# Kernel tuning notes

Hardware: AMD Instinct MI355X
Metric: run time of the kernel (lower is better)

The kernel has to match this reference:

```python
import jax, jax.numpy as jnp
import numpy as np

ANCHORS = np.array([[116.0, 90.0], [156.0, 198.0], [373.0, 326.0]], dtype=np.float32)
IMAGE_SIZE = 2048.0
IGNORE_THRES = 0.5
OBJ_SCALE = 100.0
NO_OBJ_SCALE = 1.0
EPS = 1e-16
BCE_EPS = 1e-12


def _wh_iou(anchors, gwh):
    # anchors: [A,2], gwh: [T,2] -> iou [A,T]
    aw, ah = anchors[:, 0:1], anchors[:, 1:2]            # [A,1]
    gw, gh = gwh[None, :, 0], gwh[None, :, 1]            # [1,T]
    inter = jnp.minimum(aw, gw) * jnp.minimum(ah, gh)
    union = aw * ah + gw * gh - inter
    return inter / (union + EPS)


def _bbox_iou_xywh(box1, box2):
    # boxes [T,4] in (cx, cy, w, h)
    b1x1, b1x2 = box1[:, 0] - box1[:, 2] / 2, box1[:, 0] + box1[:, 2] / 2
    b1y1, b1y2 = box1[:, 1] - box1[:, 3] / 2, box1[:, 1] + box1[:, 3] / 2
    b2x1, b2x2 = box2[:, 0] - box2[:, 2] / 2, box2[:, 0] + box2[:, 2] / 2
    b2y1, b2y2 = box2[:, 1] - box2[:, 3] / 2, box2[:, 1] + box2[:, 3] / 2
    iw = jnp.clip(jnp.minimum(b1x2, b2x2) - jnp.maximum(b1x1, b2x1), 0.0)
    ih = jnp.clip(jnp.minimum(b1y2, b2y2) - jnp.maximum(b1y1, b2y1), 0.0)
    inter = iw * ih
    a1 = (b1x2 - b1x1) * (b1y2 - b1y1)
    a2 = (b2x2 - b2x1) * (b2y2 - b2y1)
    return inter / (a1 + a2 - inter + EPS)


def _masked_mean(v, m):
    return jnp.sum(v * m) / jnp.maximum(jnp.sum(m), 1.0)


def setup_inputs() -> dict:
    key = jax.random.key(0)
    k1, k2, k3 = jax.random.split(key, 3)
    B, A, G, T = 32, 3, 256, 4096
    x = jax.random.normal(k1, (B, A * 5, G, G), jnp.float32) * 0.1
    tb = jax.random.randint(k2, (T, 1), 0, B).astype(jnp.float32)
    tcls = jnp.zeros((T, 1), jnp.float32)
    txywh = jax.random.uniform(k3, (T, 4), jnp.float32, 0.02, 0.98)
    targets = jnp.concatenate([tb, tcls, txywh], axis=1)
    return {"x": x, "targets": targets}


def reference(x, targets):
    B, G = x.shape[0], x.shape[2]
    A = ANCHORS.shape[0]
    stride = IMAGE_SIZE / G

    pred = x.reshape(B, A, 5, G, G).transpose(0, 1, 3, 4, 2)  # [B,A,G,G,5]
    cx = jax.nn.sigmoid(pred[..., 0])
    cy = jax.nn.sigmoid(pred[..., 1])
    w = pred[..., 2]
    h = pred[..., 3]
    pred_conf = jax.nn.sigmoid(pred[..., 4])

    grid_x = jnp.arange(G, dtype=jnp.float32).reshape(1, 1, 1, G)
    grid_y = jnp.arange(G, dtype=jnp.float32).reshape(1, 1, G, 1)
    anchors = jnp.asarray(ANCHORS) / stride                      # [A,2]
    aw = anchors[:, 0].reshape(1, A, 1, 1)
    ah = anchors[:, 1].reshape(1, A, 1, 1)

    pred_boxes = jnp.stack(
        [grid_x + cx, grid_y + cy, jnp.exp(w) * aw, jnp.exp(h) * ah], axis=-1
    )  # [B,A,G,G,4]
    output = jnp.concatenate(
        [pred_boxes.reshape(B, -1, 4) * stride, pred_conf.reshape(B, -1, 1)], axis=-1
    )

    # ---- build_targets (YOLOv3) ----
    tbox = targets[:, 2:6] * G                                   # [T,4] grid units
    gxy, gwh = tbox[:, :2], tbox[:, 2:]
    ious = _wh_iou(anchors, gwh)                                 # [A,T]
    best_n = jnp.argmax(ious, axis=0)                            # [T]
    b = targets[:, 0].astype(jnp.int32)
    gi = jnp.clip(jnp.floor(gxy[:, 0]), 0, G - 1).astype(jnp.int32)
    gj = jnp.clip(jnp.floor(gxy[:, 1]), 0, G - 1).astype(jnp.int32)

    zeros = jnp.zeros((B, A, G, G), jnp.float32)
    obj_mask = zeros.at[b, best_n, gj, gi].set(1.0)
    no_obj_mask = jnp.ones((B, A, G, G), jnp.float32).at[b, best_n, gj, gi].set(0.0)
    aidx = jnp.arange(A)
    keep = (ious.T <= IGNORE_THRES).astype(jnp.float32)          # [T,A]
    no_obj_mask = no_obj_mask.at[
        b[:, None], aidx[None, :], gj[:, None], gi[:, None]
    ].min(keep)

    tx = zeros.at[b, best_n, gj, gi].set(gxy[:, 0] - gi.astype(jnp.float32))
    ty = zeros.at[b, best_n, gj, gi].set(gxy[:, 1] - gj.astype(jnp.float32))
    tw = zeros.at[b, best_n, gj, gi].set(jnp.log(gwh[:, 0] / anchors[best_n, 0] + EPS))
    th = zeros.at[b, best_n, gj, gi].set(jnp.log(gwh[:, 1] / anchors[best_n, 1] + EPS))
    tconf = obj_mask

    pbt = pred_boxes[b, best_n, gj, gi]                          # [T,4]
    iou_scores = zeros.at[b, best_n, gj, gi].set(_bbox_iou_xywh(pbt, tbox))

    # ---- losses ----
    loss_x = _masked_mean((cx - tx) ** 2, obj_mask)
    loss_y = _masked_mean((cy - ty) ** 2, obj_mask)
    loss_w = _masked_mean((w - tw) ** 2, obj_mask)
    loss_h = _masked_mean((h - th) ** 2, obj_mask)
    loss_bbox = loss_x + loss_y + loss_w + loss_h
    bce = -(tconf * jnp.log(pred_conf + BCE_EPS)
            + (1.0 - tconf) * jnp.log(1.0 - pred_conf + BCE_EPS))
    loss_conf_obj = _masked_mean(bce, obj_mask)
    loss_conf_no_obj = _masked_mean(bce, no_obj_mask)
    loss_conf = OBJ_SCALE * loss_conf_obj + NO_OBJ_SCALE * loss_conf_no_obj
    loss_layer = loss_bbox + loss_conf

    # ---- metrics (side-effect scalars in torch; returned stop_gradient'd) ----
    conf50 = (pred_conf > 0.5).astype(jnp.float32)
    iou50 = (iou_scores > 0.5).astype(jnp.float32)
    iou75 = (iou_scores > 0.75).astype(jnp.float32)
    detected = conf50 * tconf
    conf_obj = _masked_mean(pred_conf, obj_mask)
    conf_no_obj = _masked_mean(pred_conf, no_obj_mask)
    precision = jnp.sum(iou50 * detected) / (jnp.sum(conf50) + EPS)
    recall50 = jnp.sum(iou50 * detected) / (jnp.sum(obj_mask) + EPS)
    recall75 = jnp.sum(iou75 * detected) / (jnp.sum(obj_mask) + EPS)
    metrics = jax.lax.stop_gradient(jnp.stack([
        loss_x, loss_y, loss_w, loss_h, loss_bbox, loss_conf, loss_layer,
        conf_obj, conf_no_obj, precision, recall50, recall75,
    ]))
    return output, loss_layer, metrics
```

## Files before the change

### kernel.cpp

```cpp
#include <hip/hip_runtime.h>
#include <cmath>

#define NA 3
#define HSIZE 8192
#define HMASK (HSIZE - 1)

typedef float v4f __attribute__((ext_vector_type(4)));


__device__ __forceinline__ float sigf(float v){ return 1.0f/(1.0f + expf(-v)); }
__device__ __forceinline__ float fast_sig(float v){
  return __builtin_amdgcn_rcpf(1.0f + __expf(-v));
}
__device__ __forceinline__ unsigned hslot(unsigned key){
  return (key * 2654435761u) >> 19;
}

__global__ __launch_bounds__(256) void k_zero(int* __restrict__ p, int n){
  int i = blockIdx.x*256 + threadIdx.x;
  if (i < n) p[i] = 0;
}

__global__ __launch_bounds__(256) void k_targets(
    const float* __restrict__ targets, int T, int G, float stride,
    int* __restrict__ ocell, int* __restrict__ keyarr,
    int* __restrict__ A_key, int* __restrict__ A_val,
    int* __restrict__ B_key, int* __restrict__ B_bits, int* __restrict__ B_maxt)
{
  int t = blockIdx.x*256 + threadIdx.x;
  if (t >= T) return;
  const float* tr = targets + (size_t)t*6;
  int b = (int)tr[0];
  float gx = tr[2]*(float)G, gy = tr[3]*(float)G, gw = tr[4]*(float)G, gh = tr[5]*(float)G;
  float aw[NA] = {116.0f/stride, 156.0f/stride, 373.0f/stride};
  float ah[NA] = { 90.0f/stride, 198.0f/stride, 326.0f/stride};
  float best_iou = -1.0f; int best = 0; int bits = 0;
  #pragma unroll
  for (int a = 0; a < NA; ++a){
    float inter = fminf(aw[a], gw) * fminf(ah[a], gh);
    float uni   = aw[a]*ah[a] + gw*gh - inter;
    float iou   = inter / (uni + 1e-16f);
    if (iou > best_iou){ best_iou = iou; best = a; }
    if (iou > 0.5f) bits |= (1 << a);
  }
  bits |= (1 << best);
  int gi = (int)floorf(gx); gi = gi < 0 ? 0 : (gi > G-1 ? G-1 : gi);
  int gj = (int)floorf(gy); gj = gj < 0 ? 0 : (gj > G-1 ? G-1 : gj);
  int cell = (b*G + gj)*G + gi;
  int okey = cell*4 + best;
  ocell[t]  = okey;
  keyarr[t] = (cell << 3) | bits;

  unsigned s = hslot((unsigned)okey) & HMASK;
  for (;;){
    int prev = atomicCAS(&A_key[s], 0, okey+1);
    if (prev == 0 || prev == okey+1){ atomicMax(&A_val[s], t+1); break; }
    s = (s+1) & HMASK;
  }
  s = hslot((unsigned)cell) & HMASK;
  for (;;){
    int prev = atomicCAS(&B_key[s], 0, cell+1);
    if (prev == 0 || prev == cell+1){
      atomicOr(&B_bits[s], bits);
      atomicMax(&B_maxt[s], t+1);
      break;
    }
    s = (s+1) & HMASK;
  }
}

__global__ __launch_bounds__(256) void k_main(
    const float* __restrict__ x, const float* __restrict__ targets,
    float* __restrict__ out, double* __restrict__ sums,
    int T, int G, float stride, int total_cells, int nblkT,
    const int* __restrict__ ocell, const int* __restrict__ keyarr,
    const int* __restrict__ A_key, const int* __restrict__ A_val,
    const int* __restrict__ B_key, const int* __restrict__ B_bits,
    const int* __restrict__ B_maxt)
{
  __shared__ float lds[256*41];
  __shared__ double sred[4][12];
  int tid = threadIdx.x;
  int lane = tid & 63, wv = tid >> 6;

  if ((int)blockIdx.x < nblkT){
    int t = blockIdx.x*256 + tid;
    double v[12];
    #pragma unroll
    for (int k = 0; k < 12; ++k) v[k] = 0.0;

    if (t < T){
      const float* tr = targets + (size_t)t*6;
      int b = (int)tr[0];
      float gx = tr[2]*(float)G, gy = tr[3]*(float)G, gw = tr[4]*(float)G, gh = tr[5]*(float)G;
      int okey = ocell[t];
      int myk  = keyarr[t];
      int cell = myk >> 3;
      int best = okey & 3;
      int gi = cell % G;
      int gj = (cell / G) % G;
      int GG = G*G;

      unsigned s = hslot((unsigned)okey) & HMASK;
      while (A_key[s] != okey+1) s = (s+1) & HMASK;
      bool owner = (A_val[s] == t+1);

      if (owner){
        float awb = (best==0 ? 116.0f : (best==1 ? 156.0f : 373.0f)) / stride;
        float ahb = (best==0 ?  90.0f : (best==1 ? 198.0f : 326.0f)) / stride;
        const float* xp = x + ((size_t)(b*(NA*5) + best*5))*GG + (size_t)gj*G + gi;
        float x0 = xp[0], x1 = xp[(size_t)GG], x2 = xp[(size_t)2*GG],
              x3 = xp[(size_t)3*GG], x4 = xp[(size_t)4*GG];
        float cx = sigf(x0), cy = sigf(x1), w = x2, h = x3, conf = sigf(x4);
        float tx = gx - (float)gi, ty = gy - (float)gj;
        float tw = logf(gw/awb + 1e-16f), th = logf(gh/ahb + 1e-16f);
        v[3] = (double)((cx-tx)*(cx-tx));
        v[4] = (double)((cy-ty)*(cy-ty));
        v[5] = (double)((w-tw)*(w-tw));
        v[6] = (double)((h-th)*(h-th));
        v[7] = (double)(-logf(conf + 1e-12f));
        v[8] = (double)conf;
        float px = (float)gi + cx, py = (float)gj + cy;
        float pw = expf(w)*awb, ph = expf(h)*ahb;
        float iw = fminf(px + pw*0.5f, gx + gw*0.5f) - fmaxf(px - pw*0.5f, gx - gw*0.5f);
        float ih = fminf(py + ph*0.5f, gy + gh*0.5f) - fmaxf(py - ph*0.5f, gy - gh*0.5f);
        iw = fmaxf(iw, 0.0f); ih = fmaxf(ih, 0.0f);
        float inter = iw*ih;
        float iou = inter / (pw*ph + gw*gh - inter + 1e-16f);
        bool det = conf > 0.5f;
        v[9]  = (iou > 0.5f  && det) ? 1.0 : 0.0;
        v[10] = (iou > 0.75f && det) ? 1.0 : 0.0;
        v[11] = 1.0;
      }

      s = hslot((unsigned)cell) & HMASK;
      while (B_key[s] != cell+1) s = (s+1) & HMASK;
      if (B_maxt[s] == t+1){
        int bits = B_bits[s];
        #pragma unroll
        for (int a = 0; a < NA; ++a){
          if (bits & (1 << a)){
            float x4 = x[((size_t)(b*(NA*5) + a*5 + 4))*GG + (size_t)gj*G + gi];
            float conf = sigf(x4);
            v[0] += (double)(-logf(1.0f - conf + 1e-12f));
            v[1] += (double)conf;
            v[2] += 1.0;
          }
        }
      }
    }

    #pragma unroll
    for (int k = 0; k < 12; ++k){
      #pragma unroll
      for (int off = 32; off > 0; off >>= 1) v[k] += __shfl_down(v[k], off);
    }
    if (lane == 0){
      #pragma unroll
      for (int k = 0; k < 12; ++k) sred[wv][k] = v[k];
    }
    __syncthreads();
    if (tid < 12){
      double sm = sred[0][tid] + sred[1][tid] + sred[2][tid] + sred[3][tid];
      unsafeAtomicAdd(&sums[3 + tid], sm);
    }
  } else {
    int dblk = blockIdx.x - nblkT;
    int i = dblk*256 + tid;
    int cell = i*8;
    float nb = 0.0f, cs = 0.0f; int c50 = 0;

    if (cell < total_cells){
      int GG = G*G;
      int gx    = cell % G;
      int row   = cell / G;
      int gy    = row % G;
      int plane = row / G;
      int a     = plane % NA;
      float aw = (a==0 ? 116.0f : (a==1 ? 156.0f : 373.0f)) / stride;
      float ah = (a==0 ?  90.0f : (a==1 ? 198.0f : 326.0f)) / stride;

      size_t base = (size_t)plane*5*GG + (size_t)gy*G + gx;
      v4f p[5][2];
      #pragma unroll
      for (int c = 0; c < 5; ++c){
        const v4f* pp = (const v4f*)(x + base + (size_t)c*GG);
        p[c][0] = pp[0];
        p[c][1] = pp[1];
      }

      float* myl = lds + tid*41;
      #pragma unroll
      for (int j = 0; j < 8; ++j){
        float cx   = fast_sig(p[0][j>>2][j&3]);
        float cy   = fast_sig(p[1][j>>2][j&3]);
        float pw   = __expf(p[2][j>>2][j&3])*aw;
        float ph   = __expf(p[3][j>>2][j&3])*ah;
        float conf = fast_sig(p[4][j>>2][j&3]);
        myl[j*5+0] = ((float)(gx + j) + cx)*stride;
        myl[j*5+1] = ((float)gy + cy)*stride;
        myl[j*5+2] = pw*stride;
        myl[j*5+3] = ph*stride;
        myl[j*5+4] = conf;
        nb -= __logf(1.0f - conf + 1e-12f);
        cs += conf;
        c50 += (conf > 0.5f) ? 1 : 0;
      }
    }
    __syncthreads();

    {
      size_t waveBase = ((size_t)dblk*2048 + (size_t)wv*512)*5;
      if (waveBase < (size_t)total_cells*5){
        const float* wl = lds + (size_t)(wv*64)*41;
        #pragma unroll
        for (int c = 0; c < 10; ++c){
          int f = (c*64 + lane)*4;
          int owner = f / 40;
          int within = f - owner*40;
          const float* src = wl + owner*41 + within;
          v4f val;
          val.x = src[0]; val.y = src[1]; val.z = src[2]; val.w = src[3];
          __builtin_nontemporal_store(val, (v4f*)(out + waveBase + f));
        }
      }
    }

    float vals[3] = {nb, cs, (float)c50};
    #pragma unroll
    for (int k = 0; k < 3; ++k){
      #pragma unroll
      for (int off = 32; off > 0; off >>= 1) vals[k] += __shfl_down(vals[k], off);
    }
    if (lane == 0){
      sred[wv][0] = (double)vals[0];
      sred[wv][1] = (double)vals[1];
      sred[wv][2] = (double)vals[2];
    }
    __syncthreads();
    if (tid < 3){
      double sm = sred[0][tid] + sred[1][tid] + sred[2][tid] + sred[3][tid];
      unsafeAtomicAdd(&sums[tid], sm);
    }
  }
}

__global__ __launch_bounds__(64) void k_final(
    const double* __restrict__ sums, float* __restrict__ tail, double total_cells)
{
  if (threadIdx.x != 0) return;
  double nb_all = sums[0], conf_all = sums[1], c50_all = sums[2];
  double enb = sums[3], econf = sums[4], ecnt = sums[5];
  double lx = sums[6], ly = sums[7], lw = sums[8], lh = sums[9];
  double bce = sums[10], cobj = sums[11], i50 = sums[12], i75 = sums[13], nobj = sums[14];

  double dObj = fmax(nobj, 1.0);
  double n_noobj = total_cells - ecnt;
  double dNo  = fmax(n_noobj, 1.0);

  double loss_x = lx/dObj, loss_y = ly/dObj, loss_w = lw/dObj, loss_h = lh/dObj;
  double loss_bbox = loss_x + loss_y + loss_w + loss_h;
  double loss_conf_obj   = bce/dObj;
  double loss_conf_noobj = (nb_all - enb)/dNo;
  double loss_conf  = 100.0*loss_conf_obj + 1.0*loss_conf_noobj;
  double loss_layer = loss_bbox + loss_conf;
  double conf_obj   = cobj/dObj;
  double conf_noobj = (conf_all - econf)/dNo;
  double precision  = i50/(c50_all + 1e-16);
  double recall50   = i50/(nobj + 1e-16);
  double recall75   = i75/(nobj + 1e-16);

  tail[0]  = (float)loss_layer;
  tail[1]  = (float)loss_x;
  tail[2]  = (float)loss_y;
  tail[3]  = (float)loss_w;
  tail[4]  = (float)loss_h;
  tail[5]  = (float)loss_bbox;
  tail[6]  = (float)loss_conf;
  tail[7]  = (float)loss_layer;
  tail[8]  = (float)conf_obj;
  tail[9]  = (float)conf_noobj;
  tail[10] = (float)precision;
  tail[11] = (float)recall50;
  tail[12] = (float)recall75;
}

extern "C" void kernel_launch(void* const* d_in, const int* in_sizes, int n_in,
                              void* d_out, int out_size, void* d_ws, size_t ws_size,
                              hipStream_t stream) {
  const float* x       = (const float*)d_in[0];
  const float* targets = (const float*)d_in[1];
  float* out = (float*)d_out;

  const int B = 32;
  int GG = in_sizes[0] / (B * NA * 5);
  int G = (int)(sqrt((double)GG) + 0.5);
  int T = in_sizes[1] / 6;
  float stride = 2048.0f / (float)G;

  char* ws = (char*)d_ws;
  double* sums  = (double*)ws;
  int* A_key  = (int*)(ws + 128);
  int* A_val  = A_key + HSIZE;
  int* B_key  = A_val + HSIZE;
  int* B_bits = B_key + HSIZE;
  int* B_maxt = B_bits + HSIZE;
  int* ocell  = B_maxt + HSIZE;
  int* keyarr = ocell + T;

  int total_cells = B * NA * GG;
  int nzero = 32 + 5*HSIZE;
  int nblkZ = (nzero + 255) / 256;
  int nblkT = (T + 255) / 256;
  int nblkD = (total_cells + 2047) / 2048;

  k_zero   <<<nblkZ, 256, 0, stream>>>((int*)ws, nzero);
  k_targets<<<nblkT, 256, 0, stream>>>(targets, T, G, stride, ocell, keyarr,
                                       A_key, A_val, B_key, B_bits, B_maxt);
  k_main   <<<nblkT + nblkD, 256, 0, stream>>>(x, targets, out, sums,
                                       T, G, stride, total_cells, nblkT,
                                       ocell, keyarr,
                                       A_key, A_val, B_key, B_bits, B_maxt);
  k_final  <<<1, 64, 0, stream>>>(sums, out + (size_t)total_cells*5, (double)total_cells);
}
```

Baseline: 241.7 us.

## Split dense-cell work into two 4-cell halves with per-wave LDS staging

Each thread now handles two groups of 4 consecutive cells, 1024 cells apart, instead of 8 contiguous cells. Both groups' loads are issued up front, and each half is transposed through a smaller per-wave LDS buffer and stored in turn. The block-wide __syncthreads is replaced by wave barriers, which should cut LDS footprint, raise occupancy and make global reads more coalesced. In exchange there are more store phases, extra index arithmetic, and a reliance on wave-local synchronisation being sufficient.

```diff
diff --git a/kernel.cpp b/kernel.cpp
--- a/kernel.cpp
+++ b/kernel.cpp
@@ -78,7 +78,7 @@
     const int* __restrict__ B_key, const int* __restrict__ B_bits,
     const int* __restrict__ B_maxt)
 {
-  __shared__ float lds[256*41];
+  __shared__ float lds[4*64*21];
   __shared__ double sred[4][12];
   int tid = threadIdx.x;
   int lane = tid & 63, wv = tid >> 6;
@@ -166,39 +166,52 @@
     }
   } else {
     int dblk = blockIdx.x - nblkT;
-    int i = dblk*256 + tid;
-    int cell = i*8;
+    int GG = G*G;
+    int blockCell = dblk*2048;
+    int cellA = blockCell + tid*4;
+    int cellB = cellA + 1024;
     float nb = 0.0f, cs = 0.0f; int c50 = 0;
 
-    if (cell < total_cells){
-      int GG = G*G;
-      int gx    = cell % G;
-      int row   = cell / G;
-      int gy    = row % G;
-      int plane = row / G;
-      int a     = plane % NA;
-      float aw = (a==0 ? 116.0f : (a==1 ? 156.0f : 373.0f)) / stride;
-      float ah = (a==0 ?  90.0f : (a==1 ? 198.0f : 326.0f)) / stride;
-
-      size_t base = (size_t)plane*5*GG + (size_t)gy*G + gx;
-      v4f p[5][2];
-      #pragma unroll
-      for (int c = 0; c < 5; ++c){
-        const v4f* pp = (const v4f*)(x + base + (size_t)c*GG);
-        p[c][0] = pp[0];
-        p[c][1] = pp[1];
-      }
-
-      float* myl = lds + tid*41;
-      #pragma unroll
-      for (int j = 0; j < 8; ++j){
-        float cx   = fast_sig(p[0][j>>2][j&3]);
-        float cy   = fast_sig(p[1][j>>2][j&3]);
-        float pw   = __expf(p[2][j>>2][j&3])*aw;
-        float ph   = __expf(p[3][j>>2][j&3])*ah;
-        float conf = fast_sig(p[4][j>>2][j&3]);
-        myl[j*5+0] = ((float)(gx + j) + cx)*stride;
-        myl[j*5+1] = ((float)gy + cy)*stride;
+    bool okA = (cellA < total_cells), okB = (cellB < total_cells);
+
+    v4f a0,a1,a2,a3,a4, b0,b1,b2,b3,b4;
+    int gxA=0,gyA=0,plA=0, gxB=0,gyB=0,plB=0;
+    if (okA){
+      gxA = cellA % G; int rowA = cellA / G; gyA = rowA % G; plA = rowA / G;
+      const float* xbA = x + (size_t)plA*5*GG + (size_t)gyA*G + gxA;
+      a0 = *(const v4f*)(xbA);
+      a1 = *(const v4f*)(xbA + (size_t)GG);
+      a2 = *(const v4f*)(xbA + (size_t)2*GG);
+      a3 = *(const v4f*)(xbA + (size_t)3*GG);
+      a4 = *(const v4f*)(xbA + (size_t)4*GG);
+    }
+    if (okB){
+      gxB = cellB % G; int rowB = cellB / G; gyB = rowB % G; plB = rowB / G;
+      const float* xbB = x + (size_t)plB*5*GG + (size_t)gyB*G + gxB;
+      b0 = *(const v4f*)(xbB);
+      b1 = *(const v4f*)(xbB + (size_t)GG);
+      b2 = *(const v4f*)(xbB + (size_t)2*GG);
+      b3 = *(const v4f*)(xbB + (size_t)3*GG);
+      b4 = *(const v4f*)(xbB + (size_t)4*GG);
+    }
+
+    float* myl = lds + (size_t)wv*1344 + (size_t)lane*21;
+    const float* wl = lds + (size_t)wv*1344;
+    size_t totalF = (size_t)total_cells*5;
+
+    if (okA){
+      int aA = plA % NA;
+      float aw = (aA==0 ? 116.0f : (aA==1 ? 156.0f : 373.0f)) / stride;
+      float ah = (aA==0 ?  90.0f : (aA==1 ? 198.0f : 326.0f)) / stride;
+      #pragma unroll
+      for (int j = 0; j < 4; ++j){
+        float cx   = fast_sig(a0[j]);
+        float cy   = fast_sig(a1[j]);
+        float pw   = __expf(a2[j])*aw;
+        float ph   = __expf(a3[j])*ah;
+        float conf = fast_sig(a4[j]);
+        myl[j*5+0] = ((float)(gxA + j) + cx)*stride;
+        myl[j*5+1] = ((float)gyA + cy)*stride;
         myl[j*5+2] = pw*stride;
         myl[j*5+3] = ph*stride;
         myl[j*5+4] = conf;
@@ -207,21 +220,58 @@
         c50 += (conf > 0.5f) ? 1 : 0;
       }
     }
-    __syncthreads();
-
+    __builtin_amdgcn_wave_barrier();
     {
-      size_t waveBase = ((size_t)dblk*2048 + (size_t)wv*512)*5;
-      if (waveBase < (size_t)total_cells*5){
-        const float* wl = lds + (size_t)(wv*64)*41;
+      size_t outBase = (size_t)dblk*10240 + (size_t)wv*1280;
+      if (outBase < totalF){
         #pragma unroll
-        for (int c = 0; c < 10; ++c){
+        for (int c = 0; c < 5; ++c){
           int f = (c*64 + lane)*4;
-          int owner = f / 40;
-          int within = f - owner*40;
-          const float* src = wl + owner*41 + within;
+          int owner = f / 20;
+          int within = f - owner*20;
+          const float* src = wl + owner*21 + within;
           v4f val;
           val.x = src[0]; val.y = src[1]; val.z = src[2]; val.w = src[3];
-          __builtin_nontemporal_store(val, (v4f*)(out + waveBase + f));
+          __builtin_nontemporal_store(val, (v4f*)(out + outBase + f));
+        }
+      }
+    }
+    __builtin_amdgcn_wave_barrier();
+
+    if (okB){
+      int aB = plB % NA;
+      float aw = (aB==0 ? 116.0f : (aB==1 ? 156.0f : 373.0f)) / stride;
+      float ah = (aB==0 ?  90.0f : (aB==1 ? 198.0f : 326.0f)) / stride;
+      #pragma unroll
+      for (int j = 0; j < 4; ++j){
+        float cx   = fast_sig(b0[j]);
+        float cy   = fast_sig(b1[j]);
+        float pw   = __expf(b2[j])*aw;
+        float ph   = __expf(b3[j])*ah;
+        float conf = fast_sig(b4[j]);
+        myl[j*5+0] = ((float)(gxB + j) + cx)*stride;
+        myl[j*5+1] = ((float)gyB + cy)*stride;
+        myl[j*5+2] = pw*stride;
+        myl[j*5+3] = ph*stride;
+        myl[j*5+4] = conf;
+        nb -= __logf(1.0f - conf + 1e-12f);
+        cs += conf;
+        c50 += (conf > 0.5f) ? 1 : 0;
+      }
+    }
+    __builtin_amdgcn_wave_barrier();
+    {
+      size_t outBase = (size_t)dblk*10240 + 5120 + (size_t)wv*1280;
+      if (outBase < totalF){
+        #pragma unroll
+        for (int c = 0; c < 5; ++c){
+          int f = (c*64 + lane)*4;
+          int owner = f / 20;
+          int within = f - owner*20;
+          const float* src = wl + owner*21 + within;
+          v4f val;
+          val.x = src[0]; val.y = src[1]; val.z = src[2]; val.w = src[3];
+          __builtin_nontemporal_store(val, (v4f*)(out + outBase + f));
         }
       }
     }
```

Measured after the change: 246.8 us. 1.02x slower.

## Fold target hashing into a single block of the main kernel

Applied to the files above, without the earlier changes.

Removes the separate target kernel and the large zeroing launch. Block 0 of the main kernel now clears the hash tables, inserts all targets with atomics, and then evaluates the target losses over up to 4096 targets in a loop. The dense output stores also switch from nontemporal to regular stores. This cuts two launches and their serialization, but it puts all target work on one block, which may now become the critical path. Recomputing anchor matching twice adds some arithmetic, and dropping nontemporal stores may change cache behaviour.

```diff
diff --git a/kernel.cpp b/kernel.cpp
--- a/kernel.cpp
+++ b/kernel.cpp
@@ -6,6 +6,7 @@
 #define HMASK (HSIZE - 1)
 
 typedef float v4f __attribute__((ext_vector_type(4)));
+typedef int   v4i __attribute__((ext_vector_type(4)));
 
 
 __device__ __forceinline__ float sigf(float v){ return 1.0f/(1.0f + expf(-v)); }
@@ -16,110 +17,119 @@
   return (key * 2654435761u) >> 19;
 }
 
-__global__ __launch_bounds__(256) void k_zero(int* __restrict__ p, int n){
-  int i = blockIdx.x*256 + threadIdx.x;
+__global__ __launch_bounds__(64) void k_zero(int* __restrict__ p, int n){
+  int i = threadIdx.x;
   if (i < n) p[i] = 0;
-}
-
-__global__ __launch_bounds__(256) void k_targets(
-    const float* __restrict__ targets, int T, int G, float stride,
-    int* __restrict__ ocell, int* __restrict__ keyarr,
-    int* __restrict__ A_key, int* __restrict__ A_val,
-    int* __restrict__ B_key, int* __restrict__ B_bits, int* __restrict__ B_maxt)
-{
-  int t = blockIdx.x*256 + threadIdx.x;
-  if (t >= T) return;
-  const float* tr = targets + (size_t)t*6;
-  int b = (int)tr[0];
-  float gx = tr[2]*(float)G, gy = tr[3]*(float)G, gw = tr[4]*(float)G, gh = tr[5]*(float)G;
-  float aw[NA] = {116.0f/stride, 156.0f/stride, 373.0f/stride};
-  float ah[NA] = { 90.0f/stride, 198.0f/stride, 326.0f/stride};
-  float best_iou = -1.0f; int best = 0; int bits = 0;
-  #pragma unroll
-  for (int a = 0; a < NA; ++a){
-    float inter = fminf(aw[a], gw) * fminf(ah[a], gh);
-    float uni   = aw[a]*ah[a] + gw*gh - inter;
-    float iou   = inter / (uni + 1e-16f);
-    if (iou > best_iou){ best_iou = iou; best = a; }
-    if (iou > 0.5f) bits |= (1 << a);
-  }
-  bits |= (1 << best);
-  int gi = (int)floorf(gx); gi = gi < 0 ? 0 : (gi > G-1 ? G-1 : gi);
-  int gj = (int)floorf(gy); gj = gj < 0 ? 0 : (gj > G-1 ? G-1 : gj);
-  int cell = (b*G + gj)*G + gi;
-  int okey = cell*4 + best;
-  ocell[t]  = okey;
-  keyarr[t] = (cell << 3) | bits;
-
-  unsigned s = hslot((unsigned)okey) & HMASK;
-  for (;;){
-    int prev = atomicCAS(&A_key[s], 0, okey+1);
-    if (prev == 0 || prev == okey+1){ atomicMax(&A_val[s], t+1); break; }
-    s = (s+1) & HMASK;
-  }
-  s = hslot((unsigned)cell) & HMASK;
-  for (;;){
-    int prev = atomicCAS(&B_key[s], 0, cell+1);
-    if (prev == 0 || prev == cell+1){
-      atomicOr(&B_bits[s], bits);
-      atomicMax(&B_maxt[s], t+1);
-      break;
-    }
-    s = (s+1) & HMASK;
-  }
 }
 
 __global__ __launch_bounds__(256) void k_main(
     const float* __restrict__ x, const float* __restrict__ targets,
     float* __restrict__ out, double* __restrict__ sums,
-    int T, int G, float stride, int total_cells, int nblkT,
-    const int* __restrict__ ocell, const int* __restrict__ keyarr,
-    const int* __restrict__ A_key, const int* __restrict__ A_val,
-    const int* __restrict__ B_key, const int* __restrict__ B_bits,
-    const int* __restrict__ B_maxt)
+    int T, int G, float stride, int total_cells,
+    int* __restrict__ A_key, int* __restrict__ A_val,
+    int* __restrict__ B_key, int* __restrict__ B_bits,
+    int* __restrict__ B_maxt)
 {
   __shared__ float lds[256*41];
   __shared__ double sred[4][12];
   int tid = threadIdx.x;
   int lane = tid & 63, wv = tid >> 6;
 
-  if ((int)blockIdx.x < nblkT){
-    int t = blockIdx.x*256 + tid;
+  if (blockIdx.x == 0){
+    {
+      v4i z = {0,0,0,0};
+      v4i* tz = (v4i*)A_key;
+      #pragma unroll
+      for (int r = 0; r < 40; ++r)
+        tz[r*256 + tid] = z;
+    }
+    __syncthreads();
+
+    for (int r = 0; r < 16; ++r){
+      int t = r*256 + tid;
+      if (t >= T) break;
+      const float* tr = targets + (size_t)t*6;
+      int b = (int)tr[0];
+      float gx = tr[2]*(float)G, gy = tr[3]*(float)G, gw = tr[4]*(float)G, gh = tr[5]*(float)G;
+      float aw[NA] = {116.0f/stride, 156.0f/stride, 373.0f/stride};
+      float ah[NA] = { 90.0f/stride, 198.0f/stride, 326.0f/stride};
+      float best_iou = -1.0f; int best = 0; int bits = 0;
+      #pragma unroll
+      for (int a = 0; a < NA; ++a){
+        float inter = fminf(aw[a], gw) * fminf(ah[a], gh);
+        float uni   = aw[a]*ah[a] + gw*gh - inter;
+        float iou   = inter / (uni + 1e-16f);
+        if (iou > best_iou){ best_iou = iou; best = a; }
+        if (iou > 0.5f) bits |= (1 << a);
+      }
+      bits |= (1 << best);
+      int gi = (int)floorf(gx); gi = gi < 0 ? 0 : (gi > G-1 ? G-1 : gi);
+      int gj = (int)floorf(gy); gj = gj < 0 ? 0 : (gj > G-1 ? G-1 : gj);
+      int cell = (b*G + gj)*G + gi;
+      int okey = cell*4 + best;
+
+      unsigned s = hslot((unsigned)okey) & HMASK;
+      for (;;){
+        int prev = atomicCAS(&A_key[s], 0, okey+1);
+        if (prev == 0 || prev == okey+1){ atomicMax(&A_val[s], t+1); break; }
+        s = (s+1) & HMASK;
+      }
+      s = hslot((unsigned)cell) & HMASK;
+      for (;;){
+        int prev = atomicCAS(&B_key[s], 0, cell+1);
+        if (prev == 0 || prev == cell+1){
+          atomicOr(&B_bits[s], bits);
+          atomicMax(&B_maxt[s], t+1);
+          break;
+        }
+        s = (s+1) & HMASK;
+      }
+    }
+    __syncthreads();
+
     double v[12];
     #pragma unroll
     for (int k = 0; k < 12; ++k) v[k] = 0.0;
-
-    if (t < T){
+    int GG = G*G;
+    for (int r = 0; r < 16; ++r){
+      int t = r*256 + tid;
+      if (t >= T) break;
       const float* tr = targets + (size_t)t*6;
       int b = (int)tr[0];
       float gx = tr[2]*(float)G, gy = tr[3]*(float)G, gw = tr[4]*(float)G, gh = tr[5]*(float)G;
-      int okey = ocell[t];
-      int myk  = keyarr[t];
-      int cell = myk >> 3;
-      int best = okey & 3;
-      int gi = cell % G;
-      int gj = (cell / G) % G;
-      int GG = G*G;
+      float aw[NA] = {116.0f/stride, 156.0f/stride, 373.0f/stride};
+      float ah[NA] = { 90.0f/stride, 198.0f/stride, 326.0f/stride};
+      float best_iou = -1.0f; int best = 0;
+      #pragma unroll
+      for (int a = 0; a < NA; ++a){
+        float inter = fminf(aw[a], gw) * fminf(ah[a], gh);
+        float uni   = aw[a]*ah[a] + gw*gh - inter;
+        float iou   = inter / (uni + 1e-16f);
+        if (iou > best_iou){ best_iou = iou; best = a; }
+      }
+      int gi = (int)floorf(gx); gi = gi < 0 ? 0 : (gi > G-1 ? G-1 : gi);
+      int gj = (int)floorf(gy); gj = gj < 0 ? 0 : (gj > G-1 ? G-1 : gj);
+      int cell = (b*G + gj)*G + gi;
+      int okey = cell*4 + best;
 
       unsigned s = hslot((unsigned)okey) & HMASK;
       while (A_key[s] != okey+1) s = (s+1) & HMASK;
       bool owner = (A_val[s] == t+1);
 
       if (owner){
-        float awb = (best==0 ? 116.0f : (best==1 ? 156.0f : 373.0f)) / stride;
-        float ahb = (best==0 ?  90.0f : (best==1 ? 198.0f : 326.0f)) / stride;
+        float awb = aw[best], ahb = ah[best];
         const float* xp = x + ((size_t)(b*(NA*5) + best*5))*GG + (size_t)gj*G + gi;
         float x0 = xp[0], x1 = xp[(size_t)GG], x2 = xp[(size_t)2*GG],
               x3 = xp[(size_t)3*GG], x4 = xp[(size_t)4*GG];
         float cx = sigf(x0), cy = sigf(x1), w = x2, h = x3, conf = sigf(x4);
         float tx = gx - (float)gi, ty = gy - (float)gj;
         float tw = logf(gw/awb + 1e-16f), th = logf(gh/ahb + 1e-16f);
-        v[3] = (double)((cx-tx)*(cx-tx));
-        v[4] = (double)((cy-ty)*(cy-ty));
-        v[5] = (double)((w-tw)*(w-tw));
-        v[6] = (double)((h-th)*(h-th));
-        v[7] = (double)(-logf(conf + 1e-12f));
-        v[8] = (double)conf;
+        v[3] += (double)((cx-tx)*(cx-tx));
+        v[4] += (double)((cy-ty)*(cy-ty));
+        v[5] += (double)((w-tw)*(w-tw));
+        v[6] += (double)((h-th)*(h-th));
+        v[7] += (double)(-logf(conf + 1e-12f));
+        v[8] += (double)conf;
         float px = (float)gi + cx, py = (float)gj + cy;
         float pw = expf(w)*awb, ph = expf(h)*ahb;
         float iw = fminf(px + pw*0.5f, gx + gw*0.5f) - fmaxf(px - pw*0.5f, gx - gw*0.5f);
@@ -128,9 +138,9 @@
         float inter = iw*ih;
         float iou = inter / (pw*ph + gw*gh - inter + 1e-16f);
         bool det = conf > 0.5f;
-        v[9]  = (iou > 0.5f  && det) ? 1.0 : 0.0;
-        v[10] = (iou > 0.75f && det) ? 1.0 : 0.0;
-        v[11] = 1.0;
+        if (iou > 0.5f  && det) v[9]  += 1.0;
+        if (iou > 0.75f && det) v[10] += 1.0;
+        v[11] += 1.0;
       }
 
       s = hslot((unsigned)cell) & HMASK;
@@ -165,7 +175,7 @@
       unsafeAtomicAdd(&sums[3 + tid], sm);
     }
   } else {
-    int dblk = blockIdx.x - nblkT;
+    int dblk = blockIdx.x - 1;
     int i = dblk*256 + tid;
     int cell = i*8;
     float nb = 0.0f, cs = 0.0f; int c50 = 0;
@@ -221,7 +231,7 @@
           const float* src = wl + owner*41 + within;
           v4f val;
           val.x = src[0]; val.y = src[1]; val.z = src[2]; val.w = src[3];
-          __builtin_nontemporal_store(val, (v4f*)(out + waveBase + f));
+          *(v4f*)(out + waveBase + f) = val;
         }
       }
     }
@@ -305,21 +315,13 @@
   int* B_key  = A_val + HSIZE;
   int* B_bits = B_key + HSIZE;
   int* B_maxt = B_bits + HSIZE;
-  int* ocell  = B_maxt + HSIZE;
-  int* keyarr = ocell + T;
 
   int total_cells = B * NA * GG;
-  int nzero = 32 + 5*HSIZE;
-  int nblkZ = (nzero + 255) / 256;
-  int nblkT = (T + 255) / 256;
   int nblkD = (total_cells + 2047) / 2048;
 
-  k_zero   <<<nblkZ, 256, 0, stream>>>((int*)ws, nzero);
-  k_targets<<<nblkT, 256, 0, stream>>>(targets, T, G, stride, ocell, keyarr,
-                                       A_key, A_val, B_key, B_bits, B_maxt);
-  k_main   <<<nblkT + nblkD, 256, 0, stream>>>(x, targets, out, sums,
-                                       T, G, stride, total_cells, nblkT,
-                                       ocell, keyarr,
+  k_zero   <<<1, 64, 0, stream>>>((int*)ws, 32);
+  k_main   <<<1 + nblkD, 256, 0, stream>>>(x, targets, out, sums,
+                                       T, G, stride, total_cells,
                                        A_key, A_val, B_key, B_bits, B_maxt);
   k_final  <<<1, 64, 0, stream>>>(sums, out + (size_t)total_cells*5, (double)total_cells);
 }
```

Result: slower. 382.7 us (+58.3%).
